# Kernel optimization log

Hardware: AMD Instinct MI355X
Metric: run time of the kernel (lower is better)

Reference implementation:

```python
import jax, jax.numpy as jnp
import numpy as np
import math

D_MODEL = 2048
N_HEADS = 16
D_FF = 8192
SEQ = 2048
BATCH = 2
THETA = 10000.0
EPS = 1e-5


def _rope(x, pos):
    # x: [B, H, S, d_k] ; pos: [B, S] int
    d = x.shape[-1]
    inv_freq = 1.0 / (THETA ** (jnp.arange(0, d, 2, dtype=jnp.float32) / d))  # [d/2]
    ang = pos[..., None].astype(jnp.float32) * inv_freq  # [B, S, d/2]
    cos = jnp.cos(ang)[:, None, :, :, None]  # [B,1,S,d/2,1]
    sin = jnp.sin(ang)[:, None, :, :, None]
    xr = x.reshape(*x.shape[:-1], d // 2, 2)
    x1, x2 = xr[..., 0], xr[..., 1]
    rot = jnp.stack((-x2, x1), axis=-1)  # rotate pairs
    out = xr * cos + rot * sin
    return out.reshape(x.shape)


def _trunc_normal(key, shape, in_f, out_f):
    std = math.sqrt(2.0 / (in_f + out_f))
    return jax.random.truncated_normal(key, -3.0, 3.0, shape, jnp.float32) * std


def setup_inputs() -> dict:
    key = jax.random.key(0)
    ks = jax.random.split(key, 8)
    x = jax.random.normal(ks[0], (BATCH, SEQ, D_MODEL), jnp.float32)
    token_positions = jnp.sort(jax.random.randint(ks[1], (BATCH, SEQ), 0, SEQ), axis=-1)
    W_qkv = _trunc_normal(ks[2], (3 * D_MODEL, D_MODEL), D_MODEL, 3 * D_MODEL)
    W_o = _trunc_normal(ks[3], (D_MODEL, D_MODEL), D_MODEL, D_MODEL)
    W1 = _trunc_normal(ks[4], (D_FF, D_MODEL), D_MODEL, D_FF)
    W3 = _trunc_normal(ks[5], (D_FF, D_MODEL), D_MODEL, D_FF)
    W2 = _trunc_normal(ks[6], (D_MODEL, D_FF), D_FF, D_MODEL)
    g1 = jnp.ones((D_MODEL,), jnp.float32)
    g2 = jnp.ones((D_MODEL,), jnp.float32)
    return {"x": x, "token_positions": token_positions, "W_qkv": W_qkv, "W_o": W_o,
            "g1": g1, "g2": g2, "W1": W1, "W3": W3, "W2": W2}


def _rmsnorm(x, g):
    xf = x.astype(jnp.float32)
    rms = jnp.sqrt(jnp.mean(xf * xf, axis=-1, keepdims=True) + EPS)
    return (xf / rms * g).astype(x.dtype)


def reference(x, token_positions, W_qkv, W_o, g1, g2, W1, W3, W2):
    B, S, D = x.shape
    H = N_HEADS
    dk = D // H
    # --- attention sublayer ---
    h = _rmsnorm(x, g1)
    qkv = jnp.einsum('bsi,oi->bso', h, W_qkv)  # [B,S,3D]
    q, k, v = jnp.split(qkv, 3, axis=-1)
    to_heads = lambda t: t.reshape(B, S, H, dk).transpose(0, 2, 1, 3)  # [B,H,S,dk]
    q, k, v = to_heads(q), to_heads(k), to_heads(v)
    q = _rope(q, token_positions)
    k = _rope(k, token_positions)
    scores = jnp.einsum('bhnd,bhmd->bhnm', q, k) / math.sqrt(dk)  # [B,H,S,S]
    mask = jnp.tril(jnp.ones((S, S), dtype=bool))
    scores = jnp.where(mask, scores, -jnp.inf)
    attn = jax.nn.softmax(scores, axis=-1)
    o = jnp.einsum('bhnm,bhmd->bhnd', attn, v)
    o = o.transpose(0, 2, 1, 3).reshape(B, S, D)
    x = x + jnp.einsum('bsi,oi->bso', o, W_o)
    # --- SwiGLU FFN sublayer ---
    h2 = _rmsnorm(x, g2)
    x1 = jnp.einsum('bsi,oi->bso', h2, W1)
    x3 = jnp.einsum('bsi,oi->bso', h2, W3)
    x = x + jnp.einsum('bsi,oi->bso', jax.nn.silu(x1) * x3, W2)
    return x
```

## Files before the change

kernel.cpp:

```cpp
#include <hip/hip_runtime.h>

#define DEV __device__ __forceinline__

typedef __bf16 bf16x8 __attribute__((ext_vector_type(8)));
typedef float f32x4 __attribute__((ext_vector_type(4)));
typedef unsigned short u16x8 __attribute__((ext_vector_type(8)));
typedef unsigned short u16x2 __attribute__((ext_vector_type(2)));

DEV unsigned short f2bf(float f) {
  unsigned int u = __float_as_uint(f);
  u += 0x7fffu + ((u >> 16) & 1u);
  return (unsigned short)(u >> 16);
}
DEV float bf2f(unsigned short h) {
  return __uint_as_float(((unsigned int)h) << 16);
}
DEV void gload16(const void* g, void* l) {
  __builtin_amdgcn_global_load_lds(
      (const __attribute__((address_space(1))) unsigned int*)g,
      (__attribute__((address_space(3))) unsigned int*)l, 16, 0, 0);
}
DEV f32x4 mfma16(bf16x8 a, bf16x8 b, f32x4 c) {
  return __builtin_amdgcn_mfma_f32_16x16x32_bf16(a, b, c, 0, 0, 0);
}

__global__ __launch_bounds__(256) void k_cvt(const float* __restrict__ in,
                                             unsigned short* __restrict__ out, int n8) {
  const int stride = gridDim.x * 256;
  for (int i = blockIdx.x * 256 + threadIdx.x; i < n8; i += stride) {
    const float4* p = (const float4*)(in + (long)i * 8);
    const float4 a = p[0], b = p[1];
    u16x8 o = { f2bf(a.x), f2bf(a.y), f2bf(a.z), f2bf(a.w),
                f2bf(b.x), f2bf(b.y), f2bf(b.z), f2bf(b.w) };
    *(u16x8*)(out + (long)i * 8) = o;
  }
}

__global__ __launch_bounds__(256) void k_rmsnorm(const float* __restrict__ x,
                                                 const float* __restrict__ g,
                                                 unsigned short* __restrict__ out) {
  const int row = blockIdx.x;
  const int t = threadIdx.x;
  const float4* xr = (const float4*)(x + (long)row * 2048);
  const float4 a = xr[t * 2], c = xr[t * 2 + 1];
  float ss = a.x * a.x + a.y * a.y + a.z * a.z + a.w * a.w +
             c.x * c.x + c.y * c.y + c.z * c.z + c.w * c.w;
#pragma unroll
  for (int o = 32; o > 0; o >>= 1) ss += __shfl_down(ss, o);
  __shared__ float ws4[4];
  __shared__ float invs;
  if ((t & 63) == 0) ws4[t >> 6] = ss;
  __syncthreads();
  if (t == 0) invs = 1.0f / sqrtf((ws4[0] + ws4[1] + ws4[2] + ws4[3]) * (1.0f / 2048.0f) + 1e-5f);
  __syncthreads();
  const float inv = invs;
  const float4* gr = (const float4*)g;
  const float4 g0 = gr[t * 2], g1v = gr[t * 2 + 1];
  u16x8 o8 = { f2bf(a.x * inv * g0.x),  f2bf(a.y * inv * g0.y),
               f2bf(a.z * inv * g0.z),  f2bf(a.w * inv * g0.w),
               f2bf(c.x * inv * g1v.x), f2bf(c.y * inv * g1v.y),
               f2bf(c.z * inv * g1v.z), f2bf(c.w * inv * g1v.w) };
  *(u16x8*)(out + (long)row * 2048 + t * 8) = o8;
}

template <int EPI>
__global__ __launch_bounds__(512, 2) void k_gemm256(
    const unsigned short* __restrict__ A, const unsigned short* __restrict__ B,
    unsigned short* __restrict__ outBF, float* __restrict__ outF,
    const float* __restrict__ resid, const unsigned short* __restrict__ aux,
    int M, int N, int K) {
  __shared__ __align__(16) unsigned short lds[2][2][2][128][64];
  const int tid = threadIdx.x;
  const int wid = tid >> 6, lane = tid & 63;
  const int wr = wid >> 2, wc = wid & 3;
  const int fr = lane & 15, g4 = lane >> 4;

  const int nwg = gridDim.x;
  int bid = blockIdx.x;
  { int q = nwg >> 3, r = nwg & 7, xcd = bid & 7, lo = bid >> 3;
    bid = (xcd < r ? xcd * (q + 1) : r * (q + 1) + (xcd - r) * q) + lo; }
  const int nxb = N >> 8;
  const int bx = bid % nxb, by = bid / nxb;
  const int arow0 = by << 8, bcol0 = bx << 8;
  const int NT = K >> 6;

  const int srow = tid >> 3;
  const int sg = (tid & 7) ^ (srow & 7);
  const unsigned short* Asrc = A + (long)(arow0 + srow) * K + (sg << 3);
  const unsigned short* Bsrc = B + (long)(bcol0 + srow) * K + (sg << 3);

  const int posk0 = (g4 ^ (lane & 7)) << 3;
  const int posk1 = ((4 + g4) ^ (lane & 7)) << 3;

  f32x4 acc[8][4] = {};
  bf16x8 a[4][2], b0[2][2], b1[2][2];

#define SB   __builtin_amdgcn_s_barrier()
#define SCH  __builtin_amdgcn_sched_barrier(0)
#define LGKM0 asm volatile("s_waitcnt lgkmcnt(0)" ::: "memory")
#define VM2  asm volatile("s_waitcnt vmcnt(2)" ::: "memory")
#define PRIO1 __builtin_amdgcn_s_setprio(1)
#define PRIO0 __builtin_amdgcn_s_setprio(0)
#define STAGE(SRC, xs, bufi, mat, h)                                            \
  { const unsigned short* s_ = (SRC) + (long)(h) * 128 * K + (long)(xs) * 64;   \
    unsigned short* d_ = &lds[bufi][mat][h][0][0] + wid * 512;                  \
    gload16(s_, d_);                                                            \
    gload16(s_ + (long)64 * K, d_ + 4096); }
#define RD_A(mh)                                                                \
  _Pragma("unroll") for (int m_ = 0; m_ < 4; ++m_) {                            \
    const unsigned short* p_ = baseA + ((mh) * 64 + m_ * 16 + fr) * 64;         \
    a[m_][0] = *(const bf16x8*)(p_ + posk0);                                    \
    a[m_][1] = *(const bf16x8*)(p_ + posk1); }
#define RD_B(arr, nh)                                                           \
  _Pragma("unroll") for (int n_ = 0; n_ < 2; ++n_) {                            \
    const unsigned short* p_ = baseB + ((nh) * 32 + n_ * 16 + fr) * 64;         \
    arr[n_][0] = *(const bf16x8*)(p_ + posk0);                                  \
    arr[n_][1] = *(const bf16x8*)(p_ + posk1); }
#define MM(mh, nh, Bv)                                                          \
  _Pragma("unroll") for (int m_ = 0; m_ < 4; ++m_)                              \
  _Pragma("unroll") for (int n_ = 0; n_ < 2; ++n_) {                            \
    acc[(mh)*4+m_][(nh)*2+n_] = mfma16(a[m_][0], Bv[n_][0], acc[(mh)*4+m_][(nh)*2+n_]); \
    acc[(mh)*4+m_][(nh)*2+n_] = mfma16(a[m_][1], Bv[n_][1], acc[(mh)*4+m_][(nh)*2+n_]); }

  STAGE(Asrc, 0, 0, 0, 0);
  STAGE(Asrc, 0, 0, 0, 1);
  STAGE(Bsrc, 0, 0, 1, 0);
  STAGE(Bsrc, 0, 0, 1, 1);
  { const int x1p = (NT > 1) ? 1 : 0;
    STAGE(Asrc, x1p, 1, 0, 0); }
  VM2; SCH; SB; SCH;

  for (int t = 0; t < NT; ++t) {
    const unsigned short* baseA = &lds[t & 1][0][wr][0][0];
    const unsigned short* baseB = &lds[t & 1][1][wc >> 1][0][0] + (wc & 1) * 4096;
    const int x1 = (t + 1 < NT) ? t + 1 : NT - 1;
    const int x2 = (t + 2 < NT) ? t + 2 : NT - 1;
    const int bn = (t + 1) & 1, bc = t & 1;

    RD_A(0); RD_B(b0, 0);
    STAGE(Asrc, x1, bn, 0, 1);
    SCH; SB; LGKM0; SCH;
    PRIO1; MM(0, 0, b0); PRIO0;
    SCH; SB; SCH;

    RD_B(b1, 1);
    STAGE(Bsrc, x1, bn, 1, 0);
    SCH; SB; LGKM0; SCH;
    PRIO1; MM(0, 1, b1); PRIO0;
    SCH; SB; SCH;

    RD_A(1);
    STAGE(Bsrc, x1, bn, 1, 1);
    SCH; SB; LGKM0; SCH;
    PRIO1; MM(1, 1, b1); PRIO0;
    SCH; SB; SCH;

    STAGE(Asrc, x2, bc, 0, 0);
    SCH; SB; SCH;
    PRIO1; MM(1, 0, b0); PRIO0;
    VM2;
    SCH; SB; SCH;
  }
#undef SB
#undef SCH
#undef LGKM0
#undef VM2
#undef PRIO1
#undef PRIO0
#undef STAGE
#undef RD_A
#undef RD_B
#undef MM

  const int er = g4 << 2;
#pragma unroll
  for (int m = 0; m < 8; ++m) {
#pragma unroll
    for (int n = 0; n < 4; ++n) {
      const int grow = arow0 + wr * 128 + m * 16 + er;
      const int gcol = bcol0 + wc * 64 + n * 16 + fr;
#pragma unroll
      for (int r = 0; r < 4; ++r) {
        const long idx = (long)(grow + r) * N + gcol;
        const float v = acc[m][n][r];
        if constexpr (EPI == 0) {
          outBF[idx] = f2bf(v);
        } else if constexpr (EPI == 1) {
          outF[idx] = resid[idx] + v;
        } else {
          const float x1v = bf2f(aux[idx]);
          const float sl = x1v / (1.0f + __expf(-x1v));
          outBF[idx] = f2bf(sl * v);
        }
      }
    }
  }
}

__global__ __launch_bounds__(256) void k_rope(const unsigned short* __restrict__ qkv,
                                              const int* __restrict__ tp,
                                              unsigned short* __restrict__ Qh,
                                              unsigned short* __restrict__ Kh, int S) {
  const int row = blockIdx.x;
  const int b = row / S, s = row - b * S;
  const float pos = (float)tp[row];
  for (int p = threadIdx.x; p < 1024; p += 256) {
    const int h = p >> 6, j = p & 63;
    const float ang = pos * __expf((float)j * -0.14391156831212787f);
    const float cc = cosf(ang), sn = sinf(ang);
    const long ib = (long)row * 6144 + h * 128 + (j << 1);
    const float q1 = bf2f(qkv[ib]), q2 = bf2f(qkv[ib + 1]);
    const float k1 = bf2f(qkv[ib + 2048]), k2 = bf2f(qkv[ib + 2049]);
    const long ob = (((long)(b * 16 + h)) * S + s) * 128 + (j << 1);
    u16x2 qo = { f2bf(q1 * cc - q2 * sn), f2bf(q2 * cc + q1 * sn) };
    u16x2 ko = { f2bf(k1 * cc - k2 * sn), f2bf(k2 * cc + k1 * sn) };
    *(u16x2*)&Qh[ob] = qo;
    *(u16x2*)&Kh[ob] = ko;
  }
}

__global__ __launch_bounds__(256) void k_vtrans(const unsigned short* __restrict__ qkv,
                                                unsigned short* __restrict__ Vt, int S) {
  __shared__ __align__(16) unsigned short t[128 * 72];
  const int bh = blockIdx.x, b = bh >> 4, h = bh & 15;
  const int s0 = blockIdx.y << 6;
  const int tid = threadIdx.x;
#pragma unroll
  for (int it = 0; it < 4; ++it) {
    const int sl = it * 16 + (tid >> 4);
    const int c = tid & 15;
    u16x8 v = *(const u16x8*)(qkv + ((long)(b * S + s0 + sl)) * 6144 + 4096 + h * 128 + (c << 3));
#pragma unroll
    for (int jj = 0; jj < 8; ++jj) t[(c * 8 + jj) * 72 + sl] = v[jj];
  }
  __syncthreads();
  const int d = tid >> 1, half = tid & 1;
  unsigned short* dst = Vt + ((long)bh * 128 + d) * S + s0 + half * 32;
  const unsigned short* srcr = &t[d * 72 + half * 32];
#pragma unroll
  for (int u = 0; u < 4; ++u)
    *(u16x8*)(dst + u * 8) = *(const u16x8*)(srcr + u * 8);
}

__global__ __launch_bounds__(256) void k_attn(const unsigned short* __restrict__ Q,
                                              const unsigned short* __restrict__ Kh,
                                              const unsigned short* __restrict__ Vt,
                                              unsigned short* __restrict__ O, int S) {
  __shared__ __align__(16) unsigned short lds_k[64 * 128];
  __shared__ __align__(16) unsigned short lds_v[128 * 64];
  __shared__ __align__(16) unsigned short lds_p[4 * 16 * 64];
  const int bh = blockIdx.x;
  const int b = bh >> 4, h = bh & 15;
  const int qt = gridDim.y - 1 - blockIdx.y;
  const int q0 = qt << 6;
  const int tid = threadIdx.x, w = tid >> 6, lane = tid & 63;
  const int fr = lane & 15, g4 = lane >> 4;

  bf16x8 qf[4];
  {
    const unsigned short* qb = Q + ((long)bh * S + q0 + w * 16 + fr) * 128 + (g4 << 3);
#pragma unroll
    for (int kk = 0; kk < 4; ++kk) qf[kk] = *(const bf16x8*)(qb + kk * 32);
  }

  f32x4 accO[8] = {};
  float mrow[4], lrow[4];
#pragma unroll
  for (int r = 0; r < 4; ++r) { mrow[r] = -1e30f; lrow[r] = 0.f; }

  const int k_row = (w << 4) + g4;
  const int k_cb = fr << 4;
  const int v_row = (w << 5) + (lane >> 3);
  const int v_cb = (lane & 7) << 4;
  const long kbase = (long)bh * S * 128;
  const long vbase = (long)bh * 128 * S;

  const int ntile = qt + 1;
  for (int it = 0; it < ntile; ++it) {
    const int kv0 = it << 6;
#pragma unroll
    for (int j = 0; j < 4; ++j) {
      const int kr = k_row + j * 4;
      const int kc = k_cb ^ ((kr & 7) << 4);
      gload16(Kh + kbase + (long)(kv0 + kr) * 128 + (kc >> 1), &lds_k[w * 2048 + j * 512]);
      const int vr = v_row + j * 8;
      const int vc = v_cb ^ ((vr & 7) << 4);
      gload16(Vt + vbase + (long)vr * S + kv0 + (vc >> 1), &lds_v[w * 2048 + j * 512]);
    }
    __syncthreads();

    f32x4 sc[4] = {};
#pragma unroll
    for (int n = 0; n < 4; ++n) {
      const int krw = n * 16 + fr;
      const int swz = (krw & 7) << 4;
#pragma unroll
      for (int kk = 0; kk < 4; ++kk) {
        const int kb = (kk << 6) + (g4 << 4);
        bf16x8 kf = *(const bf16x8*)&lds_k[krw * 128 + ((kb ^ swz) >> 1)];
        sc[n] = mfma16(qf[kk], kf, sc[n]);
      }
    }

    const float scl = 0.08838834764831845f;
    float sv[4][4];
    const bool needmask = (kv0 + 63 > q0 + w * 16);
#pragma unroll
    for (int n = 0; n < 4; ++n)
#pragma unroll
      for (int r = 0; r < 4; ++r) {
        float v = sc[n][r] * scl;
        if (needmask) {
          const int qi = q0 + w * 16 + (g4 << 2) + r;
          const int ki = kv0 + n * 16 + fr;
          if (ki > qi) v = -1e30f;
        }
        sv[n][r] = v;
      }
    float corr[4];
#pragma unroll
    for (int r = 0; r < 4; ++r) {
      float tm = fmaxf(fmaxf(sv[0][r], sv[1][r]), fmaxf(sv[2][r], sv[3][r]));
      tm = fmaxf(tm, __shfl_xor(tm, 1));
      tm = fmaxf(tm, __shfl_xor(tm, 2));
      tm = fmaxf(tm, __shfl_xor(tm, 4));
      tm = fmaxf(tm, __shfl_xor(tm, 8));
      const float mn = fmaxf(mrow[r], tm);
      corr[r] = __expf(mrow[r] - mn);
      mrow[r] = mn;
    }
    float rs[4] = {0.f, 0.f, 0.f, 0.f};
#pragma unroll
    for (int n = 0; n < 4; ++n)
#pragma unroll
      for (int r = 0; r < 4; ++r) {
        const float p = __expf(sv[n][r] - mrow[r]);
        rs[r] += p;
        const int pr = (g4 << 2) + r;
        const int pc = (n * 16 + fr) << 1;
        lds_p[(w << 10) + pr * 64 + ((pc ^ ((pr & 7) << 4)) >> 1)] = f2bf(p);
      }
#pragma unroll
    for (int r = 0; r < 4; ++r) {
      float s = rs[r];
      s += __shfl_xor(s, 1);
      s += __shfl_xor(s, 2);
      s += __shfl_xor(s, 4);
      s += __shfl_xor(s, 8);
      lrow[r] = lrow[r] * corr[r] + s;
    }
#pragma unroll
    for (int cb = 0; cb < 8; ++cb)
#pragma unroll
      for (int r = 0; r < 4; ++r) accO[cb][r] *= corr[r];

#pragma unroll
    for (int kk = 0; kk < 2; ++kk) {
      const int pb = (kk << 6) + (g4 << 4);
      bf16x8 pf = *(const bf16x8*)&lds_p[(w << 10) + fr * 64 + ((pb ^ ((fr & 7) << 4)) >> 1)];
#pragma unroll
      for (int cb = 0; cb < 8; ++cb) {
        const int vrw = cb * 16 + fr;
        bf16x8 vf = *(const bf16x8*)&lds_v[vrw * 64 + ((pb ^ ((vrw & 7) << 4)) >> 1)];
        accO[cb] = mfma16(pf, vf, accO[cb]);
      }
    }
    __syncthreads();
  }

#pragma unroll
  for (int cb = 0; cb < 8; ++cb)
#pragma unroll
    for (int r = 0; r < 4; ++r) {
      const int si = q0 + w * 16 + (g4 << 2) + r;
      const float o = accO[cb][r] / lrow[r];
      O[((long)b * S + si) * 2048 + h * 128 + cb * 16 + fr] = f2bf(o);
    }
}

extern "C" void kernel_launch(void* const* d_in, const int* in_sizes, int n_in,
                              void* d_out, int out_size, void* d_ws, size_t ws_size,
                              hipStream_t stream) {
  const float* x    = (const float*)d_in[0];
  const int*   tp   = (const int*)d_in[1];
  const float* Wqkv = (const float*)d_in[2];
  const float* Wo   = (const float*)d_in[3];
  const float* g1   = (const float*)d_in[4];
  const float* g2   = (const float*)d_in[5];
  const float* W1   = (const float*)d_in[6];
  const float* W3   = (const float*)d_in[7];
  const float* W2   = (const float*)d_in[8];
  float* out = (float*)d_out;

  char* ws = (char*)d_ws;
  const size_t MB = 1024 * 1024;
  unsigned short* Qh      = (unsigned short*)(ws + 0 * MB);
  unsigned short* Kh      = (unsigned short*)(ws + 16 * MB);
  unsigned short* Vt      = (unsigned short*)(ws + 32 * MB);
  unsigned short* O_bf    = (unsigned short*)(ws + 48 * MB);
  unsigned short* t_bf    = (unsigned short*)(ws + 0 * MB);
  unsigned short* qkv_bf  = (unsigned short*)(ws + 64 * MB);
  float*          x2      = (float*)         (ws + 64 * MB);
  unsigned short* h2_bf   = (unsigned short*)(ws + 96 * MB);
  unsigned short* wo_bf   = (unsigned short*)(ws + 96 * MB);
  unsigned short* wqkv_bf = (unsigned short*)(ws + 112 * MB);
  unsigned short* w1_bf   = (unsigned short*)(ws + 112 * MB);
  unsigned short* w2_bf   = (unsigned short*)(ws + 112 * MB);
  unsigned short* h1_bf   = (unsigned short*)(ws + 144 * MB);
  unsigned short* w3_bf   = (unsigned short*)(ws + 144 * MB);

  const int S = 2048;

  k_cvt<<<1024, 256, 0, stream>>>(Wqkv, wqkv_bf, 12582912 / 8);
  k_rmsnorm<<<4096, 256, 0, stream>>>(x, g1, h1_bf);
  k_gemm256<0><<<dim3(384), 512, 0, stream>>>(h1_bf, wqkv_bf, qkv_bf, nullptr, nullptr, nullptr, 4096, 6144, 2048);
  k_rope<<<4096, 256, 0, stream>>>(qkv_bf, tp, Qh, Kh, S);
  k_vtrans<<<dim3(32, 32), 256, 0, stream>>>(qkv_bf, Vt, S);
  k_cvt<<<1024, 256, 0, stream>>>(Wo, wo_bf, 4194304 / 8);
  k_cvt<<<1024, 256, 0, stream>>>(W1, w1_bf, 16777216 / 8);
  k_cvt<<<1024, 256, 0, stream>>>(W3, w3_bf, 16777216 / 8);
  k_attn<<<dim3(32, 32), 256, 0, stream>>>(Qh, Kh, Vt, O_bf, S);
  k_gemm256<1><<<dim3(128), 512, 0, stream>>>(O_bf, wo_bf, nullptr, x2, x, nullptr, 4096, 2048, 2048);

  k_rmsnorm<<<4096, 256, 0, stream>>>(x2, g2, h2_bf);
  k_gemm256<0><<<dim3(512), 512, 0, stream>>>(h2_bf, w1_bf, t_bf, nullptr, nullptr, nullptr, 4096, 8192, 2048);
  k_cvt<<<1024, 256, 0, stream>>>(W2, w2_bf, 16777216 / 8);
  k_gemm256<2><<<dim3(512), 512, 0, stream>>>(h2_bf, w3_bf, t_bf, nullptr, nullptr, t_bf, 4096, 8192, 2048);
  k_gemm256<1><<<dim3(128), 512, 0, stream>>>(t_bf, w2_bf, nullptr, out, x2, nullptr, 4096, 2048, 8192);
}
```

Baseline: 830.7 us.

## Add 256x128-tile GEMM with triple-buffered LDS for N=2048 output projections

```diff
diff --git a/kernel.cpp b/kernel.cpp
--- a/kernel.cpp
+++ b/kernel.cpp
@@ -23,6 +23,12 @@
 DEV f32x4 mfma16(bf16x8 a, bf16x8 b, f32x4 c) {
   return __builtin_amdgcn_mfma_f32_16x16x32_bf16(a, b, c, 0, 0, 0);
 }
+
+#define SB   __builtin_amdgcn_s_barrier()
+#define SCH  __builtin_amdgcn_sched_barrier(0)
+#define LGKM0 asm volatile("s_waitcnt lgkmcnt(0)" ::: "memory")
+#define PRIO1 __builtin_amdgcn_s_setprio(1)
+#define PRIO0 __builtin_amdgcn_s_setprio(0)
 
 __global__ __launch_bounds__(256) void k_cvt(const float* __restrict__ in,
                                              unsigned short* __restrict__ out, int n8) {
@@ -95,12 +101,7 @@
   f32x4 acc[8][4] = {};
   bf16x8 a[4][2], b0[2][2], b1[2][2];
 
-#define SB   __builtin_amdgcn_s_barrier()
-#define SCH  __builtin_amdgcn_sched_barrier(0)
-#define LGKM0 asm volatile("s_waitcnt lgkmcnt(0)" ::: "memory")
 #define VM2  asm volatile("s_waitcnt vmcnt(2)" ::: "memory")
-#define PRIO1 __builtin_amdgcn_s_setprio(1)
-#define PRIO0 __builtin_amdgcn_s_setprio(0)
 #define STAGE(SRC, xs, bufi, mat, h)                                            \
   { const unsigned short* s_ = (SRC) + (long)(h) * 128 * K + (long)(xs) * 64;   \
     unsigned short* d_ = &lds[bufi][mat][h][0][0] + wid * 512;                  \
@@ -161,12 +162,7 @@
     VM2;
     SCH; SB; SCH;
   }
-#undef SB
-#undef SCH
-#undef LGKM0
 #undef VM2
-#undef PRIO1
-#undef PRIO0
 #undef STAGE
 #undef RD_A
 #undef RD_B
@@ -192,6 +188,106 @@
           const float sl = x1v / (1.0f + __expf(-x1v));
           outBF[idx] = f2bf(sl * v);
         }
+      }
+    }
+  }
+}
+
+__global__ __launch_bounds__(512, 1) void k_gemm_n128(
+    const unsigned short* __restrict__ A, const unsigned short* __restrict__ B,
+    float* __restrict__ outF, const float* __restrict__ resid, int M, int N, int K) {
+  __shared__ __align__(16) unsigned short lds[3][384 * 64];
+  const int tid = threadIdx.x;
+  const int wid = tid >> 6, lane = tid & 63;
+  const int wr = wid >> 1, wc = wid & 1;
+  const int fr = lane & 15, g4 = lane >> 4;
+
+  const int nwg = gridDim.x;
+  int bid = blockIdx.x;
+  { int q = nwg >> 3, r = nwg & 7, xcd = bid & 7, lo = bid >> 3;
+    bid = (xcd < r ? xcd * (q + 1) : r * (q + 1) + (xcd - r) * q) + lo; }
+  const int nxb = N >> 7;
+  const int bx = bid % nxb, by = bid / nxb;
+  const int arow0 = by << 8, bcol0 = bx << 7;
+  const int NT = K >> 6;
+
+  const int srow = tid >> 3;
+  const int sg = (tid & 7) ^ (srow & 7);
+  const unsigned short* Asrc = A + (long)(arow0 + srow) * K + (sg << 3);
+  const unsigned short* Bsrc = B + (long)(bcol0 + srow) * K + (sg << 3);
+
+  const int posk0 = (g4 ^ (lane & 7)) << 3;
+  const int posk1 = ((4 + g4) ^ (lane & 7)) << 3;
+
+  f32x4 acc[4][4] = {};
+  bf16x8 a[4][2], bl[2][2], bh[2][2];
+
+#define VM6 asm volatile("s_waitcnt vmcnt(6)" ::: "memory")
+#define SITE_A(xs, bufi, s)                                                    \
+  gload16(Asrc + (long)((s) * 64) * K + (long)(xs) * 64,                       \
+          &lds[bufi][(s) * 4096] + wid * 512);
+#define SITE_B(xs, bufi, s)                                                    \
+  gload16(Bsrc + (long)((s) * 64) * K + (long)(xs) * 64,                       \
+          &lds[bufi][16384 + (s) * 4096] + wid * 512);
+#define RDA                                                                    \
+  _Pragma("unroll") for (int m_ = 0; m_ < 4; ++m_) {                           \
+    const unsigned short* p_ = bufb + (wr * 64 + m_ * 16 + fr) * 64;           \
+    a[m_][0] = *(const bf16x8*)(p_ + posk0);                                   \
+    a[m_][1] = *(const bf16x8*)(p_ + posk1); }
+#define RDB(arr, off)                                                          \
+  _Pragma("unroll") for (int n_ = 0; n_ < 2; ++n_) {                           \
+    const unsigned short* p_ = bufb + 16384 + (wc * 64 + (off) + n_ * 16 + fr) * 64; \
+    arr[n_][0] = *(const bf16x8*)(p_ + posk0);                                 \
+    arr[n_][1] = *(const bf16x8*)(p_ + posk1); }
+#define MMN(nh, Bv)                                                            \
+  _Pragma("unroll") for (int m_ = 0; m_ < 4; ++m_)                             \
+  _Pragma("unroll") for (int n_ = 0; n_ < 2; ++n_) {                           \
+    acc[m_][(nh)*2+n_] = mfma16(a[m_][0], Bv[n_][0], acc[m_][(nh)*2+n_]);      \
+    acc[m_][(nh)*2+n_] = mfma16(a[m_][1], Bv[n_][1], acc[m_][(nh)*2+n_]); }
+
+  SITE_A(0, 0, 0); SITE_A(0, 0, 1); SITE_A(0, 0, 2); SITE_A(0, 0, 3);
+  SITE_B(0, 0, 0); SITE_B(0, 0, 1);
+  { const int x1p = (NT > 1) ? 1 : 0;
+    SITE_A(x1p, 1, 0); SITE_A(x1p, 1, 1); SITE_A(x1p, 1, 2); SITE_A(x1p, 1, 3);
+    SITE_B(x1p, 1, 0); SITE_B(x1p, 1, 1); }
+  VM6; SCH; SB; SCH;
+
+  for (int t = 0; t < NT; ++t) {
+    const unsigned short* bufb = lds[t % 3];
+    const int bn = (t + 2) % 3;
+    const int xs = (t + 2 < NT) ? t + 2 : NT - 1;
+
+    RDA; RDB(bl, 0);
+    SITE_A(xs, bn, 0); SITE_A(xs, bn, 1);
+    SCH; SB; LGKM0; SCH;
+    PRIO1; MMN(0, bl); PRIO0;
+    SCH; SB; SCH;
+
+    RDB(bh, 32);
+    SITE_A(xs, bn, 2); SITE_A(xs, bn, 3); SITE_B(xs, bn, 0); SITE_B(xs, bn, 1);
+    SCH; SB; LGKM0; SCH;
+    PRIO1; MMN(1, bh); PRIO0;
+    VM6;
+    SCH; SB; SCH;
+  }
+#undef VM6
+#undef SITE_A
+#undef SITE_B
+#undef RDA
+#undef RDB
+#undef MMN
+
+  const int er = g4 << 2;
+#pragma unroll
+  for (int m = 0; m < 4; ++m) {
+#pragma unroll
+    for (int n = 0; n < 4; ++n) {
+      const int grow = arow0 + wr * 64 + m * 16 + er;
+      const int gcol = bcol0 + wc * 64 + n * 16 + fr;
+#pragma unroll
+      for (int r = 0; r < 4; ++r) {
+        const long idx = (long)(grow + r) * N + gcol;
+        outF[idx] = resid[idx] + acc[m][n][r];
       }
     }
   }
@@ -420,11 +516,11 @@
   k_cvt<<<1024, 256, 0, stream>>>(W1, w1_bf, 16777216 / 8);
   k_cvt<<<1024, 256, 0, stream>>>(W3, w3_bf, 16777216 / 8);
   k_attn<<<dim3(32, 32), 256, 0, stream>>>(Qh, Kh, Vt, O_bf, S);
-  k_gemm256<1><<<dim3(128), 512, 0, stream>>>(O_bf, wo_bf, nullptr, x2, x, nullptr, 4096, 2048, 2048);
+  k_gemm_n128<<<dim3(256), 512, 0, stream>>>(O_bf, wo_bf, x2, x, 4096, 2048, 2048);
 
   k_rmsnorm<<<4096, 256, 0, stream>>>(x2, g2, h2_bf);
   k_gemm256<0><<<dim3(512), 512, 0, stream>>>(h2_bf, w1_bf, t_bf, nullptr, nullptr, nullptr, 4096, 8192, 2048);
   k_cvt<<<1024, 256, 0, stream>>>(W2, w2_bf, 16777216 / 8);
   k_gemm256<2><<<dim3(512), 512, 0, stream>>>(h2_bf, w3_bf, t_bf, nullptr, nullptr, t_bf, 4096, 8192, 2048);
-  k_gemm256<1><<<dim3(128), 512, 0, stream>>>(t_bf, w2_bf, nullptr, out, x2, nullptr, 4096, 2048, 8192);
-}
+  k_gemm_n128<<<dim3(256), 512, 0, stream>>>(t_bf, w2_bf, out, x2, 4096, 2048, 8192);
+}
```

Measured after the change: 745.4 us. 1.11x faster.

## Split-K the N=2048 GEMMs and restructure the GEMM pipeline into paired K-steps

Applied to the files above, without the earlier changes.

```diff
diff --git a/kernel.cpp b/kernel.cpp
--- a/kernel.cpp
+++ b/kernel.cpp
@@ -23,6 +23,14 @@
 DEV f32x4 mfma16(bf16x8 a, bf16x8 b, f32x4 c) {
   return __builtin_amdgcn_mfma_f32_16x16x32_bf16(a, b, c, 0, 0, 0);
 }
+
+#define SB    __builtin_amdgcn_s_barrier()
+#define SCH   __builtin_amdgcn_sched_barrier(0)
+#define LGKM0 asm volatile("s_waitcnt lgkmcnt(0)" ::: "memory")
+#define LGKM8 asm volatile("s_waitcnt lgkmcnt(8)" ::: "memory")
+#define VM4   asm volatile("s_waitcnt vmcnt(4)" ::: "memory")
+#define PRIO1 __builtin_amdgcn_s_setprio(1)
+#define PRIO0 __builtin_amdgcn_s_setprio(0)
 
 __global__ __launch_bounds__(256) void k_cvt(const float* __restrict__ in,
                                              unsigned short* __restrict__ out, int n8) {
@@ -33,6 +41,17 @@
     u16x8 o = { f2bf(a.x), f2bf(a.y), f2bf(a.z), f2bf(a.w),
                 f2bf(b.x), f2bf(b.y), f2bf(b.z), f2bf(b.w) };
     *(u16x8*)(out + (long)i * 8) = o;
+  }
+}
+
+__global__ __launch_bounds__(256) void k_add(float* __restrict__ out,
+                                             const float* __restrict__ p, int n4) {
+  const int stride = gridDim.x * 256;
+  for (int i = blockIdx.x * 256 + threadIdx.x; i < n4; i += stride) {
+    float4 a = ((const float4*)out)[i];
+    const float4 b = ((const float4*)p)[i];
+    a.x += b.x; a.y += b.y; a.z += b.z; a.w += b.w;
+    ((float4*)out)[i] = a;
   }
 }
 
@@ -68,7 +87,7 @@
     const unsigned short* __restrict__ A, const unsigned short* __restrict__ B,
     unsigned short* __restrict__ outBF, float* __restrict__ outF,
     const float* __restrict__ resid, const unsigned short* __restrict__ aux,
-    int M, int N, int K) {
+    float* __restrict__ partial, int M, int N, int K, int Keff) {
   __shared__ __align__(16) unsigned short lds[2][2][2][128][64];
   const int tid = threadIdx.x;
   const int wid = tid >> 6, lane = tid & 63;
@@ -79,15 +98,18 @@
   int bid = blockIdx.x;
   { int q = nwg >> 3, r = nwg & 7, xcd = bid & 7, lo = bid >> 3;
     bid = (xcd < r ? xcd * (q + 1) : r * (q + 1) + (xcd - r) * q) + lo; }
+  int tile = bid, ks = 0;
+  if constexpr (EPI == 3) { ks = bid & 1; tile = bid >> 1; }
   const int nxb = N >> 8;
-  const int bx = bid % nxb, by = bid / nxb;
+  const int bx = tile % nxb, by = tile / nxb;
   const int arow0 = by << 8, bcol0 = bx << 8;
-  const int NT = K >> 6;
+  const int NT = Keff >> 6;
+  const int NPAIR = NT >> 1;
 
   const int srow = tid >> 3;
   const int sg = (tid & 7) ^ (srow & 7);
-  const unsigned short* Asrc = A + (long)(arow0 + srow) * K + (sg << 3);
-  const unsigned short* Bsrc = B + (long)(bcol0 + srow) * K + (sg << 3);
+  const unsigned short* Asrc = A + (long)(arow0 + srow) * K + (long)ks * Keff + (sg << 3);
+  const unsigned short* Bsrc = B + (long)(bcol0 + srow) * K + (long)ks * Keff + (sg << 3);
 
   const int posk0 = (g4 ^ (lane & 7)) << 3;
   const int posk1 = ((4 + g4) ^ (lane & 7)) << 3;
@@ -95,82 +117,88 @@
   f32x4 acc[8][4] = {};
   bf16x8 a[4][2], b0[2][2], b1[2][2];
 
-#define SB   __builtin_amdgcn_s_barrier()
-#define SCH  __builtin_amdgcn_sched_barrier(0)
-#define LGKM0 asm volatile("s_waitcnt lgkmcnt(0)" ::: "memory")
-#define VM2  asm volatile("s_waitcnt vmcnt(2)" ::: "memory")
-#define PRIO1 __builtin_amdgcn_s_setprio(1)
-#define PRIO0 __builtin_amdgcn_s_setprio(0)
 #define STAGE(SRC, xs, bufi, mat, h)                                            \
   { const unsigned short* s_ = (SRC) + (long)(h) * 128 * K + (long)(xs) * 64;   \
     unsigned short* d_ = &lds[bufi][mat][h][0][0] + wid * 512;                  \
     gload16(s_, d_);                                                            \
     gload16(s_ + (long)64 * K, d_ + 4096); }
-#define RD_A(mh)                                                                \
-  _Pragma("unroll") for (int m_ = 0; m_ < 4; ++m_) {                            \
-    const unsigned short* p_ = baseA + ((mh) * 64 + m_ * 16 + fr) * 64;         \
-    a[m_][0] = *(const bf16x8*)(p_ + posk0);                                    \
-    a[m_][1] = *(const bf16x8*)(p_ + posk1); }
-#define RD_B(arr, nh)                                                           \
-  _Pragma("unroll") for (int n_ = 0; n_ < 2; ++n_) {                            \
-    const unsigned short* p_ = baseB + ((nh) * 32 + n_ * 16 + fr) * 64;         \
-    arr[n_][0] = *(const bf16x8*)(p_ + posk0);                                  \
-    arr[n_][1] = *(const bf16x8*)(p_ + posk1); }
-#define MM(mh, nh, Bv)                                                          \
+#define RD_A(bufi, mh)                                                          \
+  { const unsigned short* pA_ = &lds[bufi][0][wr][0][0];                        \
+    _Pragma("unroll") for (int m_ = 0; m_ < 4; ++m_) {                          \
+      const unsigned short* p_ = pA_ + ((mh) * 64 + m_ * 16 + fr) * 64;         \
+      a[m_][0] = *(const bf16x8*)(p_ + posk0);                                  \
+      a[m_][1] = *(const bf16x8*)(p_ + posk1); } }
+#define RD_B(bufi, arr, nh)                                                     \
+  { const unsigned short* pB_ = &lds[bufi][1][wc >> 1][0][0] + (wc & 1) * 4096; \
+    _Pragma("unroll") for (int n_ = 0; n_ < 2; ++n_) {                          \
+      const unsigned short* p_ = pB_ + ((nh) * 32 + n_ * 16 + fr) * 64;         \
+      arr[n_][0] = *(const bf16x8*)(p_ + posk0);                                \
+      arr[n_][1] = *(const bf16x8*)(p_ + posk1); } }
+#define MMQ(mh, nh, Bv)                                                         \
+  _Pragma("unroll") for (int k_ = 0; k_ < 2; ++k_)                              \
   _Pragma("unroll") for (int m_ = 0; m_ < 4; ++m_)                              \
-  _Pragma("unroll") for (int n_ = 0; n_ < 2; ++n_) {                            \
-    acc[(mh)*4+m_][(nh)*2+n_] = mfma16(a[m_][0], Bv[n_][0], acc[(mh)*4+m_][(nh)*2+n_]); \
-    acc[(mh)*4+m_][(nh)*2+n_] = mfma16(a[m_][1], Bv[n_][1], acc[(mh)*4+m_][(nh)*2+n_]); }
+  _Pragma("unroll") for (int n_ = 0; n_ < 2; ++n_)                              \
+    acc[(mh)*4+m_][(nh)*2+n_] = mfma16(a[m_][k_], Bv[n_][k_], acc[(mh)*4+m_][(nh)*2+n_]);
 
   STAGE(Asrc, 0, 0, 0, 0);
   STAGE(Asrc, 0, 0, 0, 1);
   STAGE(Bsrc, 0, 0, 1, 0);
   STAGE(Bsrc, 0, 0, 1, 1);
-  { const int x1p = (NT > 1) ? 1 : 0;
-    STAGE(Asrc, x1p, 1, 0, 0); }
-  VM2; SCH; SB; SCH;
-
-  for (int t = 0; t < NT; ++t) {
-    const unsigned short* baseA = &lds[t & 1][0][wr][0][0];
-    const unsigned short* baseB = &lds[t & 1][1][wc >> 1][0][0] + (wc & 1) * 4096;
-    const int x1 = (t + 1 < NT) ? t + 1 : NT - 1;
-    const int x2 = (t + 2 < NT) ? t + 2 : NT - 1;
-    const int bn = (t + 1) & 1, bc = t & 1;
-
-    RD_A(0); RD_B(b0, 0);
-    STAGE(Asrc, x1, bn, 0, 1);
-    SCH; SB; LGKM0; SCH;
-    PRIO1; MM(0, 0, b0); PRIO0;
-    SCH; SB; SCH;
-
-    RD_B(b1, 1);
-    STAGE(Bsrc, x1, bn, 1, 0);
-    SCH; SB; LGKM0; SCH;
-    PRIO1; MM(0, 1, b1); PRIO0;
-    SCH; SB; SCH;
-
-    RD_A(1);
-    STAGE(Bsrc, x1, bn, 1, 1);
-    SCH; SB; LGKM0; SCH;
-    PRIO1; MM(1, 1, b1); PRIO0;
-    SCH; SB; SCH;
-
-    STAGE(Asrc, x2, bc, 0, 0);
-    SCH; SB; SCH;
-    PRIO1; MM(1, 0, b0); PRIO0;
-    VM2;
-    SCH; SB; SCH;
-  }
-#undef SB
-#undef SCH
-#undef LGKM0
-#undef VM2
-#undef PRIO1
-#undef PRIO0
+  { const int t1 = (NT > 1) ? 1 : 0;
+    STAGE(Bsrc, t1, 1, 1, 0);
+    STAGE(Bsrc, t1, 1, 1, 1); }
+  VM4; SCH; SB;
+
+  for (int j = 0; j < NPAIR; ++j) {
+    const int u = j << 1;
+    const int c1 = u + 1;
+    const int c2 = (u + 2 < NT) ? u + 2 : NT - 1;
+    const int c3 = (u + 3 < NT) ? u + 3 : NT - 1;
+
+    RD_A(0, 0); RD_B(0, b0, 0);
+    STAGE(Asrc, c1, 1, 0, 0);
+    LGKM8; SB; LGKM0; SCH;
+    PRIO1; MMQ(0, 0, b0); PRIO0; SB;
+
+    RD_B(0, b1, 1);
+    STAGE(Asrc, c1, 1, 0, 1);
+    SB; LGKM0; SCH;
+    PRIO1; MMQ(0, 1, b1); PRIO0; SB;
+
+    RD_A(0, 1);
+    STAGE(Bsrc, c2, 0, 1, 0);
+    SB; LGKM0; SCH;
+    PRIO1; MMQ(1, 1, b1); PRIO0; SB;
+
+    STAGE(Bsrc, c2, 0, 1, 1);
+    SB;
+    PRIO1; MMQ(1, 0, b0); PRIO0;
+    VM4; SCH; SB;
+
+    RD_A(1, 0); RD_B(1, b0, 0);
+    STAGE(Asrc, c2, 0, 0, 0);
+    LGKM8; SB; LGKM0; SCH;
+    PRIO1; MMQ(0, 0, b0); PRIO0; SB;
+
+    RD_B(1, b1, 1);
+    STAGE(Asrc, c2, 0, 0, 1);
+    SB; LGKM0; SCH;
+    PRIO1; MMQ(0, 1, b1); PRIO0; SB;
+
+    RD_A(1, 1);
+    STAGE(Bsrc, c3, 1, 1, 0);
+    SB; LGKM0; SCH;
+    PRIO1; MMQ(1, 1, b1); PRIO0; SB;
+
+    STAGE(Bsrc, c3, 1, 1, 1);
+    SB;
+    PRIO1; MMQ(1, 0, b0); PRIO0;
+    VM4; SCH; SB;
+  }
 #undef STAGE
 #undef RD_A
 #undef RD_B
-#undef MM
+#undef MMQ
 
   const int er = g4 << 2;
 #pragma unroll
@@ -187,10 +215,13 @@
           outBF[idx] = f2bf(v);
         } else if constexpr (EPI == 1) {
           outF[idx] = resid[idx] + v;
-        } else {
+        } else if constexpr (EPI == 2) {
           const float x1v = bf2f(aux[idx]);
           const float sl = x1v / (1.0f + __expf(-x1v));
           outBF[idx] = f2bf(sl * v);
+        } else {
+          if (ks == 0) outF[idx] = resid[idx] + v;
+          else         partial[idx] = v;
         }
       }
     }
@@ -210,10 +241,10 @@
     const float cc = cosf(ang), sn = sinf(ang);
     const long ib = (long)row * 6144 + h * 128 + (j << 1);
     const float q1 = bf2f(qkv[ib]), q2 = bf2f(qkv[ib + 1]);
-    const float k1 = bf2f(qkv[ib + 2048]), k2 = bf2f(qkv[ib + 2049]);
+    const float k1 = bf2f(qkv[ib + 2048]), k2v = bf2f(qkv[ib + 2049]);
     const long ob = (((long)(b * 16 + h)) * S + s) * 128 + (j << 1);
     u16x2 qo = { f2bf(q1 * cc - q2 * sn), f2bf(q2 * cc + q1 * sn) };
-    u16x2 ko = { f2bf(k1 * cc - k2 * sn), f2bf(k2 * cc + k1 * sn) };
+    u16x2 ko = { f2bf(k1 * cc - k2v * sn), f2bf(k2v * cc + k1 * sn) };
     *(u16x2*)&Qh[ob] = qo;
     *(u16x2*)&Kh[ob] = ko;
   }
@@ -291,12 +322,12 @@
 
     f32x4 sc[4] = {};
 #pragma unroll
-    for (int n = 0; n < 4; ++n) {
-      const int krw = n * 16 + fr;
-      const int swz = (krw & 7) << 4;
-#pragma unroll
-      for (int kk = 0; kk < 4; ++kk) {
-        const int kb = (kk << 6) + (g4 << 4);
+    for (int kk = 0; kk < 4; ++kk) {
+      const int kb = (kk << 6) + (g4 << 4);
+#pragma unroll
+      for (int n = 0; n < 4; ++n) {
+        const int krw = n * 16 + fr;
+        const int swz = (krw & 7) << 4;
         bf16x8 kf = *(const bf16x8*)&lds_k[krw * 128 + ((kb ^ swz) >> 1)];
         sc[n] = mfma16(qf[kk], kf, sc[n]);
       }
@@ -407,24 +438,27 @@
   unsigned short* w1_bf   = (unsigned short*)(ws + 112 * MB);
   unsigned short* w2_bf   = (unsigned short*)(ws + 112 * MB);
   unsigned short* h1_bf   = (unsigned short*)(ws + 144 * MB);
+  float*          part    = (float*)         (ws + 144 * MB);
   unsigned short* w3_bf   = (unsigned short*)(ws + 144 * MB);
 
   const int S = 2048;
 
   k_cvt<<<1024, 256, 0, stream>>>(Wqkv, wqkv_bf, 12582912 / 8);
   k_rmsnorm<<<4096, 256, 0, stream>>>(x, g1, h1_bf);
-  k_gemm256<0><<<dim3(384), 512, 0, stream>>>(h1_bf, wqkv_bf, qkv_bf, nullptr, nullptr, nullptr, 4096, 6144, 2048);
+  k_gemm256<0><<<dim3(384), 512, 0, stream>>>(h1_bf, wqkv_bf, qkv_bf, nullptr, nullptr, nullptr, nullptr, 4096, 6144, 2048, 2048);
   k_rope<<<4096, 256, 0, stream>>>(qkv_bf, tp, Qh, Kh, S);
   k_vtrans<<<dim3(32, 32), 256, 0, stream>>>(qkv_bf, Vt, S);
   k_cvt<<<1024, 256, 0, stream>>>(Wo, wo_bf, 4194304 / 8);
   k_cvt<<<1024, 256, 0, stream>>>(W1, w1_bf, 16777216 / 8);
+  k_attn<<<dim3(32, 32), 256, 0, stream>>>(Qh, Kh, Vt, O_bf, S);
+  k_gemm256<3><<<dim3(256), 512, 0, stream>>>(O_bf, wo_bf, nullptr, x2, x, nullptr, part, 4096, 2048, 2048, 1024);
+  k_add<<<2048, 256, 0, stream>>>(x2, part, 2097152);
+
+  k_rmsnorm<<<4096, 256, 0, stream>>>(x2, g2, h2_bf);
   k_cvt<<<1024, 256, 0, stream>>>(W3, w3_bf, 16777216 / 8);
-  k_attn<<<dim3(32, 32), 256, 0, stream>>>(Qh, Kh, Vt, O_bf, S);
-  k_gemm256<1><<<dim3(128), 512, 0, stream>>>(O_bf, wo_bf, nullptr, x2, x, nullptr, 4096, 2048, 2048);
-
-  k_rmsnorm<<<4096, 256, 0, stream>>>(x2, g2, h2_bf);
-  k_gemm256<0><<<dim3(512), 512, 0, stream>>>(h2_bf, w1_bf, t_bf, nullptr, nullptr, nullptr, 4096, 8192, 2048);
+  k_gemm256<0><<<dim3(512), 512, 0, stream>>>(h2_bf, w1_bf, t_bf, nullptr, nullptr, nullptr, nullptr, 4096, 8192, 2048, 2048);
   k_cvt<<<1024, 256, 0, stream>>>(W2, w2_bf, 16777216 / 8);
-  k_gemm256<2><<<dim3(512), 512, 0, stream>>>(h2_bf, w3_bf, t_bf, nullptr, nullptr, t_bf, 4096, 8192, 2048);
-  k_gemm256<1><<<dim3(128), 512, 0, stream>>>(t_bf, w2_bf, nullptr, out, x2, nullptr, 4096, 2048, 8192);
-}
+  k_gemm256<2><<<dim3(512), 512, 0, stream>>>(h2_bf, w3_bf, t_bf, nullptr, nullptr, t_bf, nullptr, 4096, 8192, 2048, 2048);
+  k_gemm256<3><<<dim3(256), 512, 0, stream>>>(t_bf, w2_bf, nullptr, out, x2, nullptr, part, 4096, 2048, 8192, 4096);
+  k_add<<<2048, 256, 0, stream>>>(out, part, 2097152);
+}
```

After: 806.7 us. 1.03x faster.
